# Kernel optimization log

Hardware: AMD Instinct MI355X
Metric: run time of the kernel (lower is better)

## Reference

```python
import jax, jax.numpy as jnp
import numpy as np


def setup_inputs() -> dict:
    key = jax.random.key(0)
    k1, k2 = jax.random.split(key, 2)
    B, C, N, O, K = 4, 3, 8192, 64, 20
    x = jax.random.normal(k1, (B, C, N), dtype=jnp.float32)          # point cloud [B,3,N]
    W = jax.random.normal(k2, (O, 2 * C), dtype=jnp.float32) * 0.1   # 1x1 conv weight on 2C edge features
    b = jnp.zeros((O,), dtype=jnp.float32)
    return {"x": x, "W": W, "b": b, "k": K}


def _knn_idx(x, k):
    # x: [B, C, N]. Same math as torch knn(): pd = -||xi||^2 + 2 xi.xj - ||xj||^2,
    # topk of pd (largest) == k nearest neighbors.
    inner = -2.0 * jnp.einsum('bcn,bcm->bnm', x, x)      # [B,N,N]
    xx = jnp.sum(x * x, axis=1)                          # [B,N]
    pd = -xx[:, :, None] - inner - xx[:, None, :]        # [B,N,N] negative sq-dist
    _, idx = jax.lax.top_k(pd, k)                        # [B,N,k]
    return idx


def reference(x, W, b, k):
    # Faithful jax version of knn + get_graph_feature + 1x1 conv + LeakyReLU + max over k
    # (DGCNN EdgeConv layer, the hot path of the encoder).
    B, C, N = x.shape
    idx = _knn_idx(x, k)                                  # [B,N,k]
    xt = jnp.transpose(x, (0, 2, 1))                      # [B,N,C]
    nb = xt[jnp.arange(B)[:, None, None], idx]            # gather neighbors [B,N,k,C]
    cen = xt[:, :, None, :]                               # [B,N,1,C]
    feat = jnp.concatenate(
        [nb - cen, jnp.broadcast_to(cen, (B, N, k, C))], axis=-1)  # [B,N,k,2C]
    h = jnp.einsum('bnkc,oc->bonk', feat, W) + b[None, :, None, None]  # [B,O,N,k]
    h = jax.nn.leaky_relu(h, negative_slope=0.2)
    return jnp.max(h, axis=-1)                            # [B,O,N]
```

## Files before the change

kernel.cpp:

```cpp
#include <hip/hip_runtime.h>
#include <cstdint>
#include <climits>

#pragma clang fp contract(off)

#define N_PTS 8192
#define B_SZ  4
#define K_NN  20
#define O_CH  64
#define QW    64
#define NSW   7
#define SUBL  1170
#define WARM  96
#define CAP   8
#define SPAD  9
#define NCH   6

typedef unsigned long long u64k;

__device__ __forceinline__ float pd_np(float qx, float qy, float qz, float xxn,
                                       float cx, float cy, float cz, float xm) {
  float p0 = qx * cx;
  float p1 = qy * cy;
  float p2 = qz * cz;
  float dot = (p0 + p1) + p2;
  float t = __builtin_fmaf(dot, 2.0f, -xxn);
  return t - xm;
}

__device__ __forceinline__ void insert20(float (&arr)[K_NN], float v) {
  float c = v;
#pragma unroll
  for (int u = K_NN - 1; u >= 0; --u) {
    float hi = fmaxf(arr[u], c);
    c = fminf(arr[u], c);
    arr[u] = hi;
  }
}

__device__ __forceinline__ void insK(u64k (&a)[K_NN], u64k k) {
  u64k c = k;
#pragma unroll
  for (int u = K_NN - 1; u >= 0; --u) {
    bool g = a[u] > c;
    u64k hi = g ? a[u] : c;
    u64k lo = g ? c : a[u];
    a[u] = hi;
    c = lo;
  }
}

__device__ __forceinline__ unsigned sortable32(float pd) {
  unsigned s = __float_as_uint(pd);
  return s ^ ((unsigned)((int)s >> 31) | 0x80000000u);
}

__device__ __forceinline__ u64k packKey(float pd, int j) {
  return ((u64k)sortable32(pd) << 13) | (unsigned)(8191 - j);
}

__device__ __forceinline__ float keyPd(u64k k) {
  unsigned sp = (unsigned)(k >> 13);
  unsigned s = (sp & 0x80000000u) ? (sp & 0x7FFFFFFFu) : ~sp;
  return __uint_as_float(s);
}

__global__ __launch_bounds__(256, 2)
void pack_kernel(const float* __restrict__ x, float4* __restrict__ P) {
  int idx = blockIdx.x * 256 + threadIdx.x;
  if (idx >= B_SZ * N_PTS) return;
  int b = idx >> 13;
  int n = idx & (N_PTS - 1);
  const float* xb = x + (size_t)b * 3 * N_PTS;
  float x0 = xb[n];
  float x1 = xb[n + N_PTS];
  float x2 = xb[n + 2 * N_PTS];
  float xxv = (x0 * x0 + x1 * x1) + x2 * x2;
  P[idx] = make_float4(x0, x1, x2, xxv);
}

__global__ __launch_bounds__(512, 4)
void knn_edgeconv_kernel(const float4* __restrict__ P,
                         const float* __restrict__ W,
                         const float* __restrict__ bias,
                         float* __restrict__ out) {
  __shared__ u64k  stk[2 * NSW * 64 * SPAD];
  __shared__ int   cnt2[2][NSW * 64];
  __shared__ short of2[2][NSW * 64];
  __shared__ float tau_l[QW];
  __shared__ int   list_l[QW][21];

  const int t  = threadIdx.x;
  const int ql = t & 63;
  const int s  = t >> 6;
  const int wb = blockIdx.x;
  const int b  = wb >> 7;
  const int n0 = (wb & 127) << 6;
  const int q  = n0 + ql;

  const float4* __restrict__ Pb = P + (size_t)b * N_PTS;

  const float4 qc = Pb[q];
  const float qx = qc.x, qy = qc.y, qz = qc.z, xxn = qc.w;

  const int sw   = __builtin_amdgcn_readfirstlane(s);
  const int j0   = (sw - 1) * SUBL;
  const int LEN  = (sw == 7) ? (N_PTS - 6 * SUBL) : SUBL;
  const int tid7 = ((sw - 1) << 6) | ql;
  const int CB[NCH + 1] = {0, 96, 192, 320, 512, 800, SUBL};

  float arrv[K_NN];
#pragma unroll
  for (int i = 0; i < K_NN; ++i) arrv[i] = -__builtin_inff();
  if (s >= 1) {
    for (int jj = 0; jj < WARM; ++jj) {
      int j = j0 + jj;
      float4 cd = Pb[j];
      float pd = pd_np(qx, qy, qz, xxn, cd.x, cd.y, cd.z, cd.w);
      if (pd > arrv[0]) insert20(arrv, pd);
    }
    float* WV = (float*)stk;
#pragma unroll
    for (int i = 0; i < K_NN; ++i) WV[tid7 * 21 + i] = arrv[i];
  }
  __syncthreads();

  u64k karr[K_NN];
#pragma unroll
  for (int i = 0; i < K_NN; ++i) karr[i] = 0ULL;
  if (s == 0) {
    const float* WV = (const float*)stk;
    for (int p = 0; p < NSW; ++p) {
      const float* pv = WV + ((p << 6) + t) * 21;
      for (int i = 0; i < K_NN; ++i) {
        float v = pv[i];
        if (v > arrv[0]) insert20(arrv, v);
      }
    }
    tau_l[t] = arrv[0];
  }
  __syncthreads();

#define PUSH(pdv, jv)                                          \
  if ((pdv) >= tau) {                                          \
    if (cnt < CAP) { my[cnt] = packKey((pdv), (jv)); ++cnt; }  \
    else if (ofj < 0) ofj = (jv);                              \
  }

  for (int st = 0; st <= NCH; ++st) {
    if (s >= 1 && st < NCH) {
      const int c = st;
      const float tau = tau_l[ql];
      int cnt = 0, ofj = -1;
      const int jb = j0 + CB[c];
      const int je = j0 + ((c == NCH - 1) ? LEN : CB[c + 1]);
      u64k* my = stk + (size_t)(c & 1) * (NSW * 64 * SPAD) + (size_t)tid7 * SPAD;
      int j = jb;
      for (; j + 3 < je; j += 4) {
        float4 d0 = Pb[j];
        float4 d1 = Pb[j + 1];
        float4 d2 = Pb[j + 2];
        float4 d3 = Pb[j + 3];
        float pd0 = pd_np(qx, qy, qz, xxn, d0.x, d0.y, d0.z, d0.w);
        float pd1 = pd_np(qx, qy, qz, xxn, d1.x, d1.y, d1.z, d1.w);
        float pd2 = pd_np(qx, qy, qz, xxn, d2.x, d2.y, d2.z, d2.w);
        float pd3 = pd_np(qx, qy, qz, xxn, d3.x, d3.y, d3.z, d3.w);
        PUSH(pd0, j)
        PUSH(pd1, j + 1)
        PUSH(pd2, j + 2)
        PUSH(pd3, j + 3)
      }
      for (; j < je; ++j) {
        float4 d0 = Pb[j];
        float pd0 = pd_np(qx, qy, qz, xxn, d0.x, d0.y, d0.z, d0.w);
        PUSH(pd0, j)
      }
      cnt2[c & 1][tid7] = cnt;
      of2[c & 1][tid7]  = (short)ofj;
    }
    if (s == 0 && st >= 1) {
      const int c = st - 1;
      const float tauc = tau_l[t];
      const u64k* sb = stk + (size_t)(c & 1) * (NSW * 64 * SPAD);
      for (int p = 0; p < NSW; ++p) {
        const int pt = (p << 6) + t;
        int pc = cnt2[c & 1][pt];
        const u64k* ps = sb + (size_t)pt * SPAD;
        for (int i = 0; i < pc; ++i) {
          u64k k = ps[i];
          if (k > karr[0]) insK(karr, k);
        }
      }
      for (int p = 0; p < NSW; ++p) {
        const int pt = (p << 6) + t;
        int oj = of2[c & 1][pt];
        if (oj >= 0) {
          int je_abs = p * SUBL +
              ((c == NCH - 1) ? ((p == NSW - 1) ? (N_PTS - 6 * SUBL) : SUBL)
                              : CB[c + 1]);
          for (int j = oj; j < je_abs; ++j) {
            float4 cd = Pb[j];
            float pdv = pd_np(qx, qy, qz, xxn, cd.x, cd.y, cd.z, cd.w);
            if (pdv >= tauc) {
              u64k k = packKey(pdv, j);
              if (k > karr[0]) insK(karr, k);
            }
          }
        }
      }
      float t20 = keyPd(karr[0]);
      tau_l[t] = fmaxf(tauc, t20);
    }
    __syncthreads();
  }
#undef PUSH

  if (s == 0) {
#pragma unroll
    for (int i = 0; i < K_NN; ++i)
      list_l[t][i] = 8191 - (int)(karr[i] & 8191ULL);
  }
  __syncthreads();

  float acc[8];
#pragma unroll
  for (int oi = 0; oi < 8; ++oi) acc[oi] = -__builtin_inff();
  const int o0 = s * 8;
  const float* __restrict__ Wp = W + o0 * 6;

  for (int nb = 0; nb < K_NN; ++nb) {
    int m = list_l[ql][nb] & (N_PTS - 1);
    float4 cm = Pb[m];
    float dx = cm.x - qx;
    float dy = cm.y - qy;
    float dz = cm.z - qz;
#pragma unroll
    for (int oi = 0; oi < 8; ++oi) {
      float h = __builtin_fmaf(dz, Wp[oi * 6 + 2],
                __builtin_fmaf(dy, Wp[oi * 6 + 1], dx * Wp[oi * 6 + 0]));
      acc[oi] = fmaxf(acc[oi], h);
    }
  }

#pragma unroll
  for (int oi = 0; oi < 8; ++oi) {
    int o = o0 + oi;
    float base = __builtin_fmaf(qz, Wp[oi * 6 + 5],
                 __builtin_fmaf(qy, Wp[oi * 6 + 4], qx * Wp[oi * 6 + 3])) + bias[o];
    float v = acc[oi] + base;
    v = fmaxf(v, 0.2f * v);
    out[((size_t)(b * O_CH + o) << 13) + q] = v;
  }
}

extern "C" void kernel_launch(void* const* d_in, const int* in_sizes, int n_in,
                              void* d_out, int out_size, void* d_ws, size_t ws_size,
                              hipStream_t stream) {
  const float* x    = (const float*)d_in[0];
  const float* W    = (const float*)d_in[1];
  const float* bias = (const float*)d_in[2];
  float4* P  = (float4*)d_ws;
  float* out = (float*)d_out;

  pack_kernel<<<dim3((B_SZ * N_PTS + 255) / 256), dim3(256), 0, stream>>>(x, P);
  knn_edgeconv_kernel<<<dim3(B_SZ * (N_PTS / QW)), dim3(512), 0, stream>>>(P, W, bias, out);
}
```

Baseline: 355.4 us.

## Branchless candidate push with double-buffered 8-wide loads and full-chunk overflow rescan

```diff
diff --git a/kernel.cpp b/kernel.cpp
--- a/kernel.cpp
+++ b/kernel.cpp
@@ -1,6 +1,5 @@
 #include <hip/hip_runtime.h>
 #include <cstdint>
-#include <climits>
 
 #pragma clang fp contract(off)
 
@@ -86,7 +85,6 @@
                          float* __restrict__ out) {
   __shared__ u64k  stk[2 * NSW * 64 * SPAD];
   __shared__ int   cnt2[2][NSW * 64];
-  __shared__ short of2[2][NSW * 64];
   __shared__ float tau_l[QW];
   __shared__ int   list_l[QW][21];
 
@@ -98,6 +96,9 @@
   const int n0 = (wb & 127) << 6;
   const int q  = n0 + ql;
 
+  int vz;
+  asm volatile("v_mov_b32 %0, 0" : "=v"(vz));
+
   const float4* __restrict__ Pb = P + (size_t)b * N_PTS;
 
   const float4 qc = Pb[q];
@@ -113,9 +114,10 @@
 #pragma unroll
   for (int i = 0; i < K_NN; ++i) arrv[i] = -__builtin_inff();
   if (s >= 1) {
+#pragma unroll 4
     for (int jj = 0; jj < WARM; ++jj) {
       int j = j0 + jj;
-      float4 cd = Pb[j];
+      float4 cd = Pb[j + vz];
       float pd = pd_np(qx, qy, qz, xxn, cd.x, cd.y, cd.z, cd.w);
       if (pd > arrv[0]) insert20(arrv, pd);
     }
@@ -141,42 +143,57 @@
   }
   __syncthreads();
 
-#define PUSH(pdv, jv)                                          \
-  if ((pdv) >= tau) {                                          \
-    if (cnt < CAP) { my[cnt] = packKey((pdv), (jv)); ++cnt; }  \
-    else if (ofj < 0) ofj = (jv);                              \
-  }
+#define PROC1(d, jv) {                                                   \
+    float pdv = pd_np(qx, qy, qz, xxn, (d).x, (d).y, (d).z, (d).w);      \
+    int slot = cnt < CAP ? cnt : CAP;                                    \
+    my[slot] = ((u64k)__float_as_uint(pdv) << 32) | (unsigned)(jv);      \
+    cnt += (pdv >= tau) ? 1 : 0;                                         \
+  }
+#define LOAD8(v, base)                                                   \
+    v##0 = Pb[(base) + 0 + vz]; v##1 = Pb[(base) + 1 + vz];              \
+    v##2 = Pb[(base) + 2 + vz]; v##3 = Pb[(base) + 3 + vz];              \
+    v##4 = Pb[(base) + 4 + vz]; v##5 = Pb[(base) + 5 + vz];              \
+    v##6 = Pb[(base) + 6 + vz]; v##7 = Pb[(base) + 7 + vz];
+#define PROC8(v, base)                                                   \
+    PROC1(v##0, (base) + 0) PROC1(v##1, (base) + 1)                      \
+    PROC1(v##2, (base) + 2) PROC1(v##3, (base) + 3)                      \
+    PROC1(v##4, (base) + 4) PROC1(v##5, (base) + 5)                      \
+    PROC1(v##6, (base) + 6) PROC1(v##7, (base) + 7)
 
   for (int st = 0; st <= NCH; ++st) {
     if (s >= 1 && st < NCH) {
       const int c = st;
       const float tau = tau_l[ql];
-      int cnt = 0, ofj = -1;
+      int cnt = 0;
       const int jb = j0 + CB[c];
       const int je = j0 + ((c == NCH - 1) ? LEN : CB[c + 1]);
       u64k* my = stk + (size_t)(c & 1) * (NSW * 64 * SPAD) + (size_t)tid7 * SPAD;
       int j = jb;
-      for (; j + 3 < je; j += 4) {
-        float4 d0 = Pb[j];
-        float4 d1 = Pb[j + 1];
-        float4 d2 = Pb[j + 2];
-        float4 d3 = Pb[j + 3];
-        float pd0 = pd_np(qx, qy, qz, xxn, d0.x, d0.y, d0.z, d0.w);
-        float pd1 = pd_np(qx, qy, qz, xxn, d1.x, d1.y, d1.z, d1.w);
-        float pd2 = pd_np(qx, qy, qz, xxn, d2.x, d2.y, d2.z, d2.w);
-        float pd3 = pd_np(qx, qy, qz, xxn, d3.x, d3.y, d3.z, d3.w);
-        PUSH(pd0, j)
-        PUSH(pd1, j + 1)
-        PUSH(pd2, j + 2)
-        PUSH(pd3, j + 3)
+      float4 a0, a1, a2, a3, a4, a5, a6, a7;
+      float4 b0, b1, b2, b3, b4, b5, b6, b7;
+      if (j + 7 < je) {
+        LOAD8(a, j)
+        for (; j + 23 < je; j += 16) {
+          LOAD8(b, j + 8)
+          PROC8(a, j)
+          LOAD8(a, j + 16)
+          PROC8(b, j + 8)
+        }
+        if (j + 15 < je) {
+          LOAD8(b, j + 8)
+          PROC8(a, j)
+          PROC8(b, j + 8)
+          j += 16;
+        } else {
+          PROC8(a, j)
+          j += 8;
+        }
       }
       for (; j < je; ++j) {
-        float4 d0 = Pb[j];
-        float pd0 = pd_np(qx, qy, qz, xxn, d0.x, d0.y, d0.z, d0.w);
-        PUSH(pd0, j)
+        float4 d = Pb[j + vz];
+        PROC1(d, j)
       }
       cnt2[c & 1][tid7] = cnt;
-      of2[c & 1][tid7]  = (short)ofj;
     }
     if (s == 0 && st >= 1) {
       const int c = st - 1;
@@ -185,21 +202,22 @@
       for (int p = 0; p < NSW; ++p) {
         const int pt = (p << 6) + t;
         int pc = cnt2[c & 1][pt];
-        const u64k* ps = sb + (size_t)pt * SPAD;
-        for (int i = 0; i < pc; ++i) {
-          u64k k = ps[i];
-          if (k > karr[0]) insK(karr, k);
-        }
-      }
-      for (int p = 0; p < NSW; ++p) {
-        const int pt = (p << 6) + t;
-        int oj = of2[c & 1][pt];
-        if (oj >= 0) {
-          int je_abs = p * SUBL +
+        if (pc <= CAP) {
+          const u64k* ps = sb + (size_t)pt * SPAD;
+          for (int i = 0; i < pc; ++i) {
+            u64k e = ps[i];
+            float pdv = __uint_as_float((unsigned)(e >> 32));
+            int jv = (int)(e & 0xFFFFFFFFu);
+            u64k k = packKey(pdv, jv);
+            if (k > karr[0]) insK(karr, k);
+          }
+        } else {
+          int jb2 = p * SUBL + CB[c];
+          int je2 = p * SUBL +
               ((c == NCH - 1) ? ((p == NSW - 1) ? (N_PTS - 6 * SUBL) : SUBL)
                               : CB[c + 1]);
-          for (int j = oj; j < je_abs; ++j) {
-            float4 cd = Pb[j];
+          for (int j = jb2; j < je2; ++j) {
+            float4 cd = Pb[j + vz];
             float pdv = pd_np(qx, qy, qz, xxn, cd.x, cd.y, cd.z, cd.w);
             if (pdv >= tauc) {
               u64k k = packKey(pdv, j);
@@ -213,7 +231,9 @@
     }
     __syncthreads();
   }
-#undef PUSH
+#undef PROC1
+#undef LOAD8
+#undef PROC8
 
   if (s == 0) {
 #pragma unroll
```

Result: slower. 994.1 us (+179.7%).
